# Performance work log

Hardware: AMD Instinct MI355X
Metric: run time of the kernel (lower is better)

The kernel has to match this reference:

```python
import jax, jax.numpy as jnp
import numpy as np

DIM = 384
HEADS = 6
HD = DIM // HEADS
PATCH = 2
FR = 0.5
HEXP = int(HEADS * 4.0)       # attn_proj expanded heads
PR = DIM // 4                  # SQA proj1 out dim
HID = DIM * 4                  # MLP hidden
EPS = 1e-5
SCALE = 1.0 / np.sqrt(HD).astype(np.float32)


def _ln(x, w, b):
    m = jnp.mean(x, axis=-1, keepdims=True)
    v = jnp.var(x, axis=-1, keepdims=True)
    return (x - m) / jnp.sqrt(v + EPS) * w + b


def _lin(x, w, b):
    return x @ w.T + b


def setup_inputs() -> dict:
    key = jax.random.key(0)
    ks = jax.random.split(key, 16)
    def p(i, shape, s=0.02):
        return jax.random.normal(ks[i], shape, jnp.float32) * s
    return {
        "x": jax.random.normal(ks[0], (3136, DIM), jnp.float32),
        "qa": jax.random.normal(ks[1], (1, DIM), jnp.float32),
        "conv_w": p(2, (DIM, 1, 3, 3), 0.1),
        "conv_b": jnp.zeros((DIM,), jnp.float32),
        "norm1_w": jnp.ones((DIM,), jnp.float32),
        "norm1_b": jnp.zeros((DIM,), jnp.float32),
        "norm2_w": jnp.ones((DIM,), jnp.float32),
        "norm2_b": jnp.zeros((DIM,), jnp.float32),
        "qkv_w": p(3, (3 * DIM, DIM)),
        "qkv_b": jnp.zeros((3 * DIM,), jnp.float32),
        "mproj_w": p(4, (DIM, DIM)),
        "mproj_b": jnp.zeros((DIM,), jnp.float32),
        "ap1_w": p(5, (HEXP, HEADS), 0.1),
        "ap1_b": jnp.zeros((HEXP,), jnp.float32),
        "ap2_w": p(6, (HEADS, HEXP), 0.1),
        "ap2_b": jnp.zeros((HEADS,), jnp.float32),
        "kv_w": p(7, (2 * DIM, DIM)),
        "kv_b": jnp.zeros((2 * DIM,), jnp.float32),
        "sp1_w": p(8, (PR, DIM)),
        "sp1_b": jnp.zeros((PR,), jnp.float32),
        "sp2_w": p(9, (DIM, PR)),
        "sp2_b": jnp.zeros((DIM,), jnp.float32),
        "pn_w": jnp.ones((PR,), jnp.float32),
        "pn_b": jnp.zeros((PR,), jnp.float32),
        "fc1_w": p(10, (HID, DIM)),
        "fc1_b": jnp.zeros((HID,), jnp.float32),
        "fc2_w": p(11, (DIM, HID)),
        "fc2_b": jnp.zeros((DIM,), jnp.float32),
    }


def _mmsa(x, qkv_w, qkv_b, mproj_w, mproj_b, ap1_w, ap1_b, ap2_w, ap2_b):
    # x: [S, DIM]
    s = x.shape[0]
    qkv = _lin(x, qkv_w, qkv_b).reshape(s, 3, HEADS, HD).transpose(1, 2, 0, 3)  # [3,h,s,d]
    q, k, v = qkv[0], qkv[1], qkv[2]
    attn = jnp.einsum('hqd,hkd->hqk', q, k) * SCALE           # [h,q,k]
    a = attn.transpose(1, 2, 0)                                # [q,k,h]
    a = a @ ap1_w.T + ap1_b                                    # [q,k,hexp]
    a = jax.nn.softmax(a, axis=1)                              # softmax over k (axis=1)
    a = a @ ap2_w.T + ap2_b                                    # [q,k,h]
    attn = a.transpose(2, 0, 1)                                # [h,q,k]
    out = jnp.einsum('hqk,hkd->hqd', attn, v)
    out = out.transpose(1, 0, 2).reshape(s, DIM)
    return _lin(out, mproj_w, mproj_b)


def _sqa(x, q, kv_w, kv_b, sp1_w, sp1_b, sp2_w, sp2_b, pn_w, pn_b):
    # x: [S, DIM], q: [1, DIM]
    s = x.shape[0]
    qh = q.reshape(1, HEADS, HD).transpose(1, 0, 2)            # [h,1,d]
    kv = _lin(x, kv_w, kv_b).reshape(s, 2, HEADS, HD).transpose(1, 2, 0, 3)
    k, v = kv[0], kv[1]
    attn = jax.nn.softmax(jnp.einsum('hqd,hkd->hqk', qh, k) * SCALE, axis=-1)
    x1 = jnp.einsum('hqk,hkd->hqd', attn, v).transpose(1, 0, 2).reshape(1, DIM)
    x1 = jax.nn.relu(_ln(_lin(x1, sp1_w, sp1_b), pn_w, pn_b))
    x1 = _lin(x1, sp2_w, sp2_b)
    return x + x1                                              # broadcast residual over S


def reference(x, qa, conv_w, conv_b, norm1_w, norm1_b, norm2_w, norm2_b,
              qkv_w, qkv_b, mproj_w, mproj_b, ap1_w, ap1_b, ap2_w, ap2_b,
              kv_w, kv_b, sp1_w, sp1_b, sp2_w, sp2_b, pn_w, pn_b,
              fc1_w, fc1_b, fc2_w, fc2_b):
    L = x.shape[0]
    Hs = int(np.sqrt(L)); Ws = Hs
    # PosCNN2D: depthwise 3x3 conv + residual
    xi = x.T.reshape(1, DIM, Hs, Ws)
    conv = jax.lax.conv_general_dilated(xi, conv_w, (1, 1), 'SAME', feature_group_count=DIM)
    xi = conv + conv_b[None, :, None, None] + xi
    c = xi[0]                                                  # [DIM,Hs,Ws]
    hp, wp = Hs // PATCH, Ws // PATCH
    # 'c (h h1) (w w1) -> (h w) (h1 w1) c'
    x1 = c.reshape(DIM, hp, PATCH, wp, PATCH).transpose(1, 3, 2, 4, 0).reshape(hp * wp, PATCH * PATCH, DIM)
    n = hp * wp
    nf = int(n * FR)
    means = x1.mean(axis=(1, 2))
    idx = jnp.argsort(-means)                                  # descending
    nf_idx, nb_idx = idx[:nf], idx[nf:]
    f = x1[nf_idx].reshape(nf * PATCH * PATCH, DIM)
    b = x1[nb_idx].reshape((n - nf) * PATCH * PATCH, DIM)
    qf = _mmsa(jnp.concatenate([qa, f], axis=0),
               qkv_w, qkv_b, mproj_w, mproj_b, ap1_w, ap1_b, ap2_w, ap2_b)
    qa2, f = qf[:1], qf[1:]
    b = _sqa(b, qa2, kv_w, kv_b, sp1_w, sp1_b, sp2_w, sp2_b, pn_w, pn_b)
    # scatter foreground/background back to patch order
    x1n = jnp.zeros_like(x1)
    x1n = x1n.at[nf_idx].set(f.reshape(nf, PATCH * PATCH, DIM))
    x1n = x1n.at[nb_idx].set(b.reshape(n - nf, PATCH * PATCH, DIM))
    # inverse rearrange '(h w) (h1 w1) c -> ((h h1)(w w1)) c'
    x1f = x1n.reshape(hp, wp, PATCH, PATCH, DIM).transpose(0, 2, 1, 3, 4).reshape(L, DIM)
    x = x + _ln(x1f, norm1_w, norm1_b)
    h = _ln(x, norm2_w, norm2_b)
    h = jax.nn.silu(_lin(h, fc1_w, fc1_b))
    x = x + _lin(h, fc2_w, fc2_b)
    return x, qa2
```

## Files before the change

### kernel.cpp

```cpp
#include <hip/hip_runtime.h>
#include <hip/hip_bf16.h>

#define DIM 384
#define HEADS 6
#define HD 64
#define LPIX 3136
#define HS 56
#define NPATCH 784
#define NF 392
#define SEQ 1569
#define BROWS 1568
#define HEXP 24
#define PR 96
#define HID 1536
#define SCALE 0.125f
#define EPSV 1e-5f
#define KPAD 1576
#define QSTR 9456

typedef short short8v __attribute__((ext_vector_type(8)));
typedef float f32x4 __attribute__((ext_vector_type(4)));
typedef unsigned short ushort;

__device__ __forceinline__ ushort f2b(float f) {
    __hip_bfloat16 h = __float2bfloat16(f);
    return reinterpret_cast<ushort&>(h);
}
__device__ __forceinline__ float b2f(ushort u) {
    unsigned int ui = ((unsigned int)u) << 16;
    return __uint_as_float(ui);
}

struct CvtSeg { const float* s; ushort* d; int n; };
__global__ __launch_bounds__(256) void cvt_kernel(CvtSeg a, CvtSeg b, CvtSeg c, CvtSeg d, CvtSeg e) {
    CvtSeg seg;
    switch (blockIdx.y) { case 0: seg = a; break; case 1: seg = b; break; case 2: seg = c; break;
                          case 3: seg = d; break; default: seg = e; break; }
    int idx = (blockIdx.x * 256 + threadIdx.x) * 8;
    if (idx >= seg.n) return;
    float4 f0 = *reinterpret_cast<const float4*>(seg.s + idx);
    float4 f1 = *reinterpret_cast<const float4*>(seg.s + idx + 4);
    ushort u[8] = { f2b(f0.x), f2b(f0.y), f2b(f0.z), f2b(f0.w),
                    f2b(f1.x), f2b(f1.y), f2b(f1.z), f2b(f1.w) };
    *reinterpret_cast<uint4*>(seg.d + idx) = *reinterpret_cast<uint4*>(u);
}

__global__ __launch_bounds__(384) void conv_kernel(const float* __restrict__ x,
                                                   const float* __restrict__ cw,
                                                   const float* __restrict__ cb,
                                                   float* __restrict__ x1,
                                                   float* __restrict__ means) {
    int l = blockIdx.x, c = threadIdx.x;
    int wid = c >> 6, lane = c & 63;
    int hh = l / HS, ww = l % HS;
    float acc = x[(long)l * DIM + c] + cb[c];
    #pragma unroll
    for (int kh = 0; kh < 3; kh++) {
        int h2 = hh + kh - 1;
        if (h2 < 0 || h2 >= HS) continue;
        #pragma unroll
        for (int kw = 0; kw < 3; kw++) {
            int w2 = ww + kw - 1;
            if (w2 < 0 || w2 >= HS) continue;
            acc += x[((long)h2 * HS + w2) * DIM + c] * cw[c * 9 + kh * 3 + kw];
        }
    }
    int p = (hh >> 1) * 28 + (ww >> 1);
    int t = ((hh & 1) << 1) | (ww & 1);
    x1[(long)(p * 4 + t) * DIM + c] = acc;
    float s = acc;
    #pragma unroll
    for (int off = 32; off >= 1; off >>= 1) s += __shfl_xor(s, off);
    __shared__ float wred[6];
    if (lane == 0) wred[wid] = s;
    __syncthreads();
    if (c == 0) atomicAdd(&means[p], wred[0] + wred[1] + wred[2] + wred[3] + wred[4] + wred[5]);
}

__global__ __launch_bounds__(1024) void partition_kernel(const float* __restrict__ means, int* __restrict__ isfg,
                                                         int* __restrict__ pos, int* __restrict__ fgmap,
                                                         int* __restrict__ bgmap) {
    __shared__ float m_s[NPATCH];
    __shared__ unsigned char flag_s[NPATCH];
    __shared__ int scan_s[256];
    int tid = threadIdx.x;
    if (tid < NPATCH) m_s[tid] = means[tid];
    __syncthreads();
    if (tid < NPATCH) {
        float m = m_s[tid];
        int rank = 0;
        for (int q2 = 0; q2 < NPATCH; q2++) {
            float mq = m_s[q2];
            rank += (mq > m) || (mq == m && q2 < tid);
        }
        flag_s[tid] = (rank < NF) ? 1 : 0;
    }
    __syncthreads();
    if (tid < 256) {
        int base = tid * 4, cnt = 0;
        #pragma unroll
        for (int i = 0; i < 4; i++) { int p = base + i; if (p < NPATCH) cnt += flag_s[p]; }
        scan_s[tid] = cnt;
    }
    __syncthreads();
    for (int off = 1; off < 256; off <<= 1) {
        int add = 0;
        if (tid < 256 && tid >= off) add = scan_s[tid - off];
        __syncthreads();
        if (tid < 256) scan_s[tid] += add;
        __syncthreads();
    }
    if (tid < 256) {
        int base = tid * 4, cnt = 0;
        #pragma unroll
        for (int i = 0; i < 4; i++) { int p = base + i; if (p < NPATCH) cnt += flag_s[p]; }
        int run = scan_s[tid] - cnt;
        for (int i = 0; i < 4; i++) {
            int p = base + i;
            if (p >= NPATCH) break;
            int f = flag_s[p];
            if (f) { isfg[p] = 1; pos[p] = run; fgmap[run] = p; run++; }
            else   { isfg[p] = 0; pos[p] = p - run; bgmap[p - run] = p; }
        }
    }
}

__global__ __launch_bounds__(384) void gather_kernel(const float* __restrict__ x1, const float* __restrict__ qa,
                                                     const int* __restrict__ fgmap, const int* __restrict__ bgmap,
                                                     ushort* __restrict__ Xmsa_bf, ushort* __restrict__ B_bf) {
    int c = threadIdx.x;
    int bid = blockIdx.x;
    if (bid == 0) { Xmsa_bf[c] = f2b(qa[c]); return; }
    if (bid <= BROWS) {
        int r = bid - 1;
        int src = fgmap[r >> 2] * 4 + (r & 3);
        Xmsa_bf[(long)bid * DIM + c] = f2b(x1[(long)src * DIM + c]);
    } else {
        int r = bid - SEQ;
        int src = bgmap[r >> 2] * 4 + (r & 3);
        B_bf[(long)r * DIM + c] = f2b(x1[(long)src * DIM + c]);
    }
}

template<int BM, int BN, int BK, int OPB, int ACT, int OUTBF>
__global__ __launch_bounds__(256) void mgemm(
    const ushort* __restrict__ A, int lda, long long sA,
    const ushort* __restrict__ B, int ldb, long long sB,
    const float* __restrict__ bias, const float* __restrict__ resid, int ldr,
    void* __restrict__ Cv, int ldc, long long sC,
    int M, int N, int K, float alpha) {
    constexpr int LDT = BK + 8;
    constexpr int WR = (BM == 128 && BN == 128) ? 2 : ((BM == 128) ? 4 : 2);
    constexpr int WC = 4 / WR;
    constexpr int MFR = BM / WR / 16;
    constexpr int NFR = BN / WC / 16;
    constexpr int KH = BK / 32;
    __shared__ ushort As[BM * LDT];
    __shared__ ushort Bs[BN * LDT];
    int tid = threadIdx.x;
    int wid = tid >> 6, lane = tid & 63;
    int m0 = blockIdx.y * BM, n0 = blockIdx.x * BN;
    int bz = blockIdx.z;
    A += (long long)bz * sA;
    B += (long long)bz * sB;
    int wm = (wid / WC) * (BM / WR);
    int wn = (wid % WC) * (BN / WC);
    f32x4 acc[MFR][NFR];
    #pragma unroll
    for (int mi = 0; mi < MFR; mi++)
        #pragma unroll
        for (int ni = 0; ni < NFR; ni++) acc[mi][ni] = (f32x4){0.f, 0.f, 0.f, 0.f};

    for (int k0 = 0; k0 < K; k0 += BK) {
        {
            constexpr int CPR = BK / 8;
            constexpr int CHA = BM * CPR / 256;
            #pragma unroll
            for (int t = 0; t < CHA; t++) {
                int chunk = tid + t * 256;
                int row = chunk / CPR, part = chunk % CPR;
                int gm = m0 + row, gk = k0 + part * 8;
                ushort* dst = &As[row * LDT + part * 8];
                if (gm < M && gk + 8 <= K) {
                    *reinterpret_cast<uint4*>(dst) =
                        *reinterpret_cast<const uint4*>(&A[(long long)gm * lda + gk]);
                } else {
                    #pragma unroll
                    for (int i = 0; i < 8; i++) {
                        int k = gk + i;
                        dst[i] = (gm < M && k < K) ? A[(long long)gm * lda + k] : (ushort)0;
                    }
                }
            }
        }
        if (OPB == 1) {
            constexpr int CPR = BK / 8;
            constexpr int CHB = BN * CPR / 256;
            #pragma unroll
            for (int t = 0; t < CHB; t++) {
                int chunk = tid + t * 256;
                int row = chunk / CPR, part = chunk % CPR;
                int gn = n0 + row, gk = k0 + part * 8;
                ushort* dst = &Bs[row * LDT + part * 8];
                if (gn < N && gk + 8 <= K) {
                    *reinterpret_cast<uint4*>(dst) =
                        *reinterpret_cast<const uint4*>(&B[(long long)gn * ldb + gk]);
                } else {
                    #pragma unroll
                    for (int i = 0; i < 8; i++) {
                        int k = gk + i;
                        dst[i] = (gn < N && k < K) ? B[(long long)gn * ldb + k] : (ushort)0;
                    }
                }
            }
        } else {
            int kr = tid >> 2, nn = (tid & 3) * 16;
            int gk = k0 + kr;
            ushort vals[16];
            if (gk < K && n0 + nn + 16 <= N) {
                *reinterpret_cast<uint4*>(vals) =
                    *reinterpret_cast<const uint4*>(&B[(long long)gk * ldb + n0 + nn]);
                *reinterpret_cast<uint4*>(vals + 8) =
                    *reinterpret_cast<const uint4*>(&B[(long long)gk * ldb + n0 + nn + 8]);
            } else {
                #pragma unroll
                for (int i = 0; i < 16; i++) {
                    int gn = n0 + nn + i;
                    vals[i] = (gk < K && gn < N) ? B[(long long)gk * ldb + gn] : (ushort)0;
                }
            }
            #pragma unroll
            for (int i = 0; i < 16; i++) Bs[(nn + i) * LDT + kr] = vals[i];
        }
        __syncthreads();
        #pragma unroll
        for (int kh = 0; kh < KH; kh++) {
            short8v a[MFR], b[NFR];
            int kcol = kh * 32 + (lane >> 4) * 8;
            #pragma unroll
            for (int mi = 0; mi < MFR; mi++)
                a[mi] = *reinterpret_cast<const short8v*>(&As[(wm + mi * 16 + (lane & 15)) * LDT + kcol]);
            #pragma unroll
            for (int ni = 0; ni < NFR; ni++)
                b[ni] = *reinterpret_cast<const short8v*>(&Bs[(wn + ni * 16 + (lane & 15)) * LDT + kcol]);
            #pragma unroll
            for (int mi = 0; mi < MFR; mi++)
                #pragma unroll
                for (int ni = 0; ni < NFR; ni++)
                    acc[mi][ni] = __builtin_amdgcn_mfma_f32_16x16x32_bf16(a[mi], b[ni], acc[mi][ni], 0, 0, 0);
        }
        __syncthreads();
    }
    ushort* C16 = (ushort*)Cv;
    float* C32 = (float*)Cv;
    #pragma unroll
    for (int mi = 0; mi < MFR; mi++) {
        #pragma unroll
        for (int j = 0; j < 4; j++) {
            int gm = m0 + wm + mi * 16 + (lane >> 4) * 4 + j;
            if (gm >= M) continue;
            #pragma unroll
            for (int ni = 0; ni < NFR; ni++) {
                int gn = n0 + wn + ni * 16 + (lane & 15);
                if (gn >= N) continue;
                float v = acc[mi][ni][j] * alpha;
                if (bias) v += bias[gn];
                if (ACT == 1) v = v / (1.f + __expf(-v));
                if (resid) v += resid[(long long)gm * ldr + gn];
                long long ci = bz * sC + (long long)gm * ldc + gn;
                if (OUTBF) C16[ci] = f2b(v); else C32[ci] = v;
            }
        }
    }
}

__global__ __launch_bounds__(512, 2) void modattn_kernel(
    ushort* __restrict__ S,
    const float* __restrict__ ap1_w, const float* __restrict__ ap1_b,
    const float* __restrict__ ap2_w, const float* __restrict__ ap2_b) {
    int q = blockIdx.x, tid = threadIdx.x;
    int wid = tid >> 6, lane = tid & 63;
    __shared__ ushort s_lds[6 * KPAD];
    __shared__ float w1s[144], w2s[144], b1s[24], b2s[6];
    __shared__ float red[8][12];
    __shared__ float fin[12];
    if (tid < 144) { w1s[tid] = ap1_w[tid]; w2s[tid] = ap2_w[tid]; }
    if (tid < 24) b1s[tid] = ap1_b[tid];
    if (tid < 6)  b2s[tid] = ap2_b[tid];
    {
        const uint4* g = reinterpret_cast<const uint4*>(S + (long long)q * QSTR);
        uint4* l = reinterpret_cast<uint4*>(s_lds);
        #pragma unroll
        for (int t = 0; t < 3; t++) {
            int i = tid + t * 512;
            if (i < 1182) l[i] = g[i];
        }
    }
    __syncthreads();
    float a2acc[4][6];
    #pragma unroll
    for (int j = 0; j < 4; j++)
        #pragma unroll
        for (int h = 0; h < 6; h++) a2acc[j][h] = b2s[h];

    #pragma unroll
    for (int c = 0; c < 2; c++) {
        float a1[4][12];
        float r12[12];
        #pragma unroll
        for (int e = 0; e < 12; e++) r12[e] = -3.4e38f;
        #pragma unroll
        for (int j = 0; j < 4; j++) {
            int k = tid + j * 512;
            bool val = k < SEQ;
            int kc = val ? k : 0;
            float sv[6];
            #pragma unroll
            for (int h = 0; h < 6; h++) sv[h] = b2f(s_lds[h * KPAD + kc]);
            #pragma unroll
            for (int e = 0; e < 12; e++) {
                int eg = c * 12 + e;
                float a = b1s[eg];
                #pragma unroll
                for (int h = 0; h < 6; h++) a = fmaf(sv[h], w1s[eg * 6 + h], a);
                a1[j][e] = a;
                if (val) r12[e] = fmaxf(r12[e], a);
            }
        }
        #pragma unroll
        for (int e = 0; e < 12; e++) {
            float v = r12[e];
            #pragma unroll
            for (int off = 32; off >= 1; off >>= 1) v = fmaxf(v, __shfl_xor(v, off));
            r12[e] = v;
        }
        if (lane == 0) {
            #pragma unroll
            for (int e = 0; e < 12; e++) red[wid][e] = r12[e];
        }
        __syncthreads();
        if (tid < 12) {
            float v = red[0][tid];
            #pragma unroll
            for (int w = 1; w < 8; w++) v = fmaxf(v, red[w][tid]);
            fin[tid] = v;
        }
        __syncthreads();
        #pragma unroll
        for (int e = 0; e < 12; e++) r12[e] = 0.f;
        #pragma unroll
        for (int j = 0; j < 4; j++) {
            int k = tid + j * 512;
            bool val = k < SEQ;
            #pragma unroll
            for (int e = 0; e < 12; e++) {
                float p = val ? __expf(a1[j][e] - fin[e]) : 0.f;
                a1[j][e] = p;
                r12[e] += p;
            }
        }
        #pragma unroll
        for (int e = 0; e < 12; e++) {
            float v = r12[e];
            #pragma unroll
            for (int off = 32; off >= 1; off >>= 1) v += __shfl_xor(v, off);
            r12[e] = v;
        }
        if (lane == 0) {
            #pragma unroll
            for (int e = 0; e < 12; e++) red[wid][e] = r12[e];
        }
        __syncthreads();
        if (tid < 12) {
            float v = red[0][tid];
            #pragma unroll
            for (int w = 1; w < 8; w++) v += red[w][tid];
            fin[tid] = 1.f / v;
        }
        __syncthreads();
        #pragma unroll
        for (int j = 0; j < 4; j++) {
            #pragma unroll
            for (int e = 0; e < 12; e++) {
                float p = a1[j][e] * fin[e];
                int eg = c * 12 + e;
                #pragma unroll
                for (int h = 0; h < 6; h++) a2acc[j][h] = fmaf(p, w2s[h * 24 + eg], a2acc[j][h]);
            }
        }
    }
    #pragma unroll
    for (int j = 0; j < 4; j++) {
        int k = tid + j * 512;
        if (k < SEQ) {
            #pragma unroll
            for (int h = 0; h < 6; h++) s_lds[h * KPAD + k] = f2b(a2acc[j][h]);
        } else if (k < KPAD) {
            #pragma unroll
            for (int h = 0; h < 6; h++) s_lds[h * KPAD + k] = 0;
        }
    }
    __syncthreads();
    {
        const uint4* l = reinterpret_cast<const uint4*>(s_lds);
        uint4* g = reinterpret_cast<uint4*>(S + (long long)q * QSTR);
        #pragma unroll
        for (int t = 0; t < 3; t++) {
            int i = tid + t * 512;
            if (i < 1182) g[i] = l[i];
        }
    }
}

__global__ __launch_bounds__(512) void sqa_attn_kernel(const float* __restrict__ kv, const float* __restrict__ qa2,
                                                       float* __restrict__ x1h) {
    int h = blockIdx.x, tid = threadIdx.x;
    int wid = tid >> 6, lane = tid & 63;
    __shared__ float q_s[HD];
    __shared__ float l_s[BROWS];
    __shared__ float red8[8];
    __shared__ float pvred[8][HD];
    __shared__ float gmv;
    if (tid < HD) q_s[tid] = qa2[h * HD + tid];
    __syncthreads();
    float lmax = -1e30f;
    #pragma unroll
    for (int j = 0; j < 4; j++) {
        int s = tid + j * 512;
        if (s < BROWS) {
            const float4* kr = reinterpret_cast<const float4*>(kv + (long long)s * 768 + h * HD);
            float d = 0.f;
            #pragma unroll
            for (int i = 0; i < 16; i++) {
                float4 f = kr[i];
                d = fmaf(f.x, q_s[i * 4 + 0], d); d = fmaf(f.y, q_s[i * 4 + 1], d);
                d = fmaf(f.z, q_s[i * 4 + 2], d); d = fmaf(f.w, q_s[i * 4 + 3], d);
            }
            d *= SCALE;
            l_s[s] = d;
            lmax = fmaxf(lmax, d);
        }
    }
    #pragma unroll
    for (int off = 32; off >= 1; off >>= 1) lmax = fmaxf(lmax, __shfl_xor(lmax, off));
    if (lane == 0) red8[wid] = lmax;
    __syncthreads();
    if (tid == 0) {
        float v = red8[0];
        #pragma unroll
        for (int w = 1; w < 8; w++) v = fmaxf(v, red8[w]);
        gmv = v;
    }
    __syncthreads();
    float gmax = gmv;
    float lsum = 0.f;
    #pragma unroll
    for (int j = 0; j < 4; j++) {
        int s = tid + j * 512;
        if (s < BROWS) { float pp = __expf(l_s[s] - gmax); l_s[s] = pp; lsum += pp; }
    }
    #pragma unroll
    for (int off = 32; off >= 1; off >>= 1) lsum += __shfl_xor(lsum, off);
    if (lane == 0) red8[wid] = lsum;
    __syncthreads();
    if (tid == 0) {
        float v = 0.f;
        #pragma unroll
        for (int w = 0; w < 8; w++) v += red8[w];
        gmv = 1.f / v;
    }
    __syncthreads();
    float inv = gmv;
    int d = tid & 63, g = tid >> 6;
    float acc = 0.f;
    for (int s = g; s < BROWS; s += 8)
        acc = fmaf(l_s[s], kv[(long long)s * 768 + 384 + h * HD + d], acc);
    pvred[g][d] = acc;
    __syncthreads();
    if (tid < HD) {
        float v = 0.f;
        #pragma unroll
        for (int w = 0; w < 8; w++) v += pvred[w][tid];
        x1h[h * HD + tid] = v * inv;
    }
}

__global__ __launch_bounds__(384) void sqa_mlp_kernel(const float* __restrict__ x1h,
                                                      const float* __restrict__ sp1_w, const float* __restrict__ sp1_b,
                                                      const float* __restrict__ pn_w, const float* __restrict__ pn_b,
                                                      const float* __restrict__ sp2_w, const float* __restrict__ sp2_b,
                                                      float* __restrict__ z,
                                                      const float* __restrict__ mp, float* __restrict__ dq) {
    __shared__ float y_s[PR];
    __shared__ float x_s[DIM];
    __shared__ float mv[2];
    int tid = threadIdx.x;
    dq[tid] = mp[tid];
    x_s[tid] = x1h[tid];
    __syncthreads();
    if (tid < PR) {
        float a = sp1_b[tid];
        for (int c = 0; c < DIM; c++) a += sp1_w[tid * DIM + c] * x_s[c];
        y_s[tid] = a;
    }
    __syncthreads();
    if (tid == 0) {
        float m = 0.f; for (int i = 0; i < PR; i++) m += y_s[i]; m /= (float)PR;
        float v = 0.f; for (int i = 0; i < PR; i++) { float d = y_s[i] - m; v += d * d; } v /= (float)PR;
        mv[0] = m; mv[1] = rsqrtf(v + EPSV);
    }
    __syncthreads();
    if (tid < PR) {
        float yn = (y_s[tid] - mv[0]) * mv[1] * pn_w[tid] + pn_b[tid];
        y_s[tid] = fmaxf(yn, 0.f);
    }
    __syncthreads();
    float a = sp2_b[tid];
    for (int j = 0; j < PR; j++) a += sp2_w[tid * PR + j] * y_s[j];
    z[tid] = a;
}

__global__ __launch_bounds__(384) void scatter_ln_kernel(
    const float* __restrict__ x, const float* __restrict__ mpout, const ushort* __restrict__ B_bf,
    const float* __restrict__ z, const int* __restrict__ isfg, const int* __restrict__ pos,
    const float* __restrict__ n1w, const float* __restrict__ n1b,
    const float* __restrict__ n2w, const float* __restrict__ n2b,
    float* __restrict__ x_mid, ushort* __restrict__ hnorm_bf) {
    int l = blockIdx.x, c = threadIdx.x;
    int wid = c >> 6, lane = c & 63;
    int hh = l / HS, ww = l % HS;
    int p = (hh >> 1) * 28 + (ww >> 1);
    int t = ((hh & 1) << 1) | (ww & 1);
    float v;
    if (isfg[p]) v = mpout[(long long)(1 + pos[p] * 4 + t) * DIM + c];
    else v = b2f(B_bf[(long long)(pos[p] * 4 + t) * DIM + c]) + z[c];
    __shared__ float r0[8], r1[8], r2[8], r3[8];
    float s1 = v, s2 = v * v;
    #pragma unroll
    for (int off = 32; off >= 1; off >>= 1) { s1 += __shfl_xor(s1, off); s2 += __shfl_xor(s2, off); }
    if (lane == 0) { r0[wid] = s1; r1[wid] = s2; }
    __syncthreads();
    float mean = (r0[0] + r0[1] + r0[2] + r0[3] + r0[4] + r0[5]) / (float)DIM;
    float var = (r1[0] + r1[1] + r1[2] + r1[3] + r1[4] + r1[5]) / (float)DIM - mean * mean;
    float xm = x[(long long)l * DIM + c] + (v - mean) * rsqrtf(var + EPSV) * n1w[c] + n1b[c];
    x_mid[(long long)l * DIM + c] = xm;
    s1 = xm; s2 = xm * xm;
    #pragma unroll
    for (int off = 32; off >= 1; off >>= 1) { s1 += __shfl_xor(s1, off); s2 += __shfl_xor(s2, off); }
    if (lane == 0) { r2[wid] = s1; r3[wid] = s2; }
    __syncthreads();
    float m2 = (r2[0] + r2[1] + r2[2] + r2[3] + r2[4] + r2[5]) / (float)DIM;
    float v2 = (r3[0] + r3[1] + r3[2] + r3[3] + r3[4] + r3[5]) / (float)DIM - m2 * m2;
    hnorm_bf[(long long)l * DIM + c] = f2b((xm - m2) * rsqrtf(v2 + EPSV) * n2w[c] + n2b[c]);
}

extern "C" void kernel_launch(void* const* d_in, const int* in_sizes, int n_in,
                              void* d_out, int out_size, void* d_ws, size_t ws_size,
                              hipStream_t stream) {
    const float* x       = (const float*)d_in[0];
    const float* qa      = (const float*)d_in[1];
    const float* conv_w  = (const float*)d_in[2];
    const float* conv_b  = (const float*)d_in[3];
    const float* n1w     = (const float*)d_in[4];
    const float* n1b     = (const float*)d_in[5];
    const float* n2w     = (const float*)d_in[6];
    const float* n2b     = (const float*)d_in[7];
    const float* qkv_w   = (const float*)d_in[8];
    const float* qkv_b   = (const float*)d_in[9];
    const float* mproj_w = (const float*)d_in[10];
    const float* mproj_b = (const float*)d_in[11];
    const float* ap1_w   = (const float*)d_in[12];
    const float* ap1_b   = (const float*)d_in[13];
    const float* ap2_w   = (const float*)d_in[14];
    const float* ap2_b   = (const float*)d_in[15];
    const float* kv_w    = (const float*)d_in[16];
    const float* kv_b    = (const float*)d_in[17];
    const float* sp1_w   = (const float*)d_in[18];
    const float* sp1_b   = (const float*)d_in[19];
    const float* sp2_w   = (const float*)d_in[20];
    const float* sp2_b   = (const float*)d_in[21];
    const float* pn_w    = (const float*)d_in[22];
    const float* pn_b    = (const float*)d_in[23];
    const float* fc1_w   = (const float*)d_in[24];
    const float* fc1_b   = (const float*)d_in[25];
    const float* fc2_w   = (const float*)d_in[26];
    const float* fc2_b   = (const float*)d_in[27];
    float* out = (float*)d_out;
    float* ws  = (float*)d_ws;

    const long long X1_OFF    = 0;
    const long long BMAT_OFF  = 1204224;
    const long long S_OFF     = 1806336;
    const long long MPOUT_OFF = 16576912;
    const long long XMID_OFF  = 17179408;
    const long long WBF_OFF   = 18383632;
    const long long MEANS_OFF = 19415824;
    const long long X1H_OFF   = 19416608;
    const long long Z_OFF     = 19416992;
    const long long ISFG_OFF  = 19418160;
    const long long POS_OFF   = 19418944;
    const long long FGMAP_OFF = 19419728;
    const long long BGMAP_OFF = 19420120;

    float*  x1_arr  = ws + X1_OFF;
    float*  mpout   = ws + MPOUT_OFF;
    float*  xmid    = ws + XMID_OFF;
    float*  means   = ws + MEANS_OFF;
    float*  x1h     = ws + X1H_OFF;
    float*  zvec    = ws + Z_OFF;
    int*    isfg    = (int*)(ws + ISFG_OFF);
    int*    pos     = (int*)(ws + POS_OFF);
    int*    fgmap   = (int*)(ws + FGMAP_OFF);
    int*    bgmap   = (int*)(ws + BGMAP_OFF);

    ushort* S16     = (ushort*)(ws + S_OFF);
    ushort* qkvb_bf = (ushort*)(ws + X1_OFF);
    ushort* Xmsa_bf = (ushort*)(ws + MPOUT_OFF);
    ushort* Bmat_bf = (ushort*)(ws + BMAT_OFF);
    ushort* attn_bf = (ushort*)(ws + XMID_OFF);
    float*  kv_out  = ws + S_OFF;
    ushort* hnorm_bf= (ushort*)(ws + S_OFF + 1204224);
    ushort* hact_bf = (ushort*)(ws + S_OFF + 1806336);

    ushort* wbf      = (ushort*)(ws + WBF_OFF);
    ushort* qkvw_bf  = wbf;
    ushort* mprojw_bf= wbf + 442368;
    ushort* kvw_bf   = wbf + 589824;
    ushort* fc1w_bf  = wbf + 884736;
    ushort* fc2w_bf  = wbf + 1474560;

    {
        CvtSeg s0{qkv_w, qkvw_bf, 442368};
        CvtSeg s1{mproj_w, mprojw_bf, 147456};
        CvtSeg s2{kv_w, kvw_bf, 294912};
        CvtSeg s3{fc1_w, fc1w_bf, 589824};
        CvtSeg s4{fc2_w, fc2w_bf, 589824};
        dim3 g(288, 5, 1);
        cvt_kernel<<<g, 256, 0, stream>>>(s0, s1, s2, s3, s4);
    }

    hipMemsetAsync(means, 0, NPATCH * sizeof(float), stream);
    conv_kernel<<<LPIX, 384, 0, stream>>>(x, conv_w, conv_b, x1_arr, means);
    partition_kernel<<<1, 1024, 0, stream>>>(means, isfg, pos, fgmap, bgmap);
    gather_kernel<<<SEQ + BROWS, 384, 0, stream>>>(x1_arr, qa, fgmap, bgmap, Xmsa_bf, Bmat_bf);

    {
        dim3 g(18, 25, 1);
        mgemm<64,64,64,1,0,1><<<g, 256, 0, stream>>>(Xmsa_bf, DIM, 0, qkvw_bf, DIM, 0, qkv_b,
                                                     nullptr, 0, qkvb_bf, 1152, 0, SEQ, 1152, DIM, 1.f);
    }
    {
        dim3 g(13, 13, 6);
        mgemm<128,128,64,1,0,1><<<g, 256, 0, stream>>>(qkvb_bf, 1152, 64, qkvb_bf + 384, 1152, 64, nullptr,
                                                       nullptr, 0, S16, QSTR, (long long)KPAD, SEQ, SEQ, HD, SCALE);
    }
    modattn_kernel<<<SEQ, 512, 0, stream>>>(S16, ap1_w, ap1_b, ap2_w, ap2_b);
    {
        dim3 g(1, 25, 6);
        mgemm<64,64,64,0,0,1><<<g, 256, 0, stream>>>(S16, QSTR, (long long)KPAD, qkvb_bf + 768, 1152, 64, nullptr,
                                                     nullptr, 0, attn_bf, DIM, 64, SEQ, HD, SEQ, 1.f);
    }
    {
        dim3 g(6, 25, 1);
        mgemm<64,64,64,1,0,0><<<g, 256, 0, stream>>>(attn_bf, DIM, 0, mprojw_bf, DIM, 0, mproj_b,
                                                     nullptr, 0, mpout, DIM, 0, SEQ, DIM, DIM, 1.f);
    }
    {
        dim3 g(12, 25, 1);
        mgemm<64,64,64,1,0,0><<<g, 256, 0, stream>>>(Bmat_bf, DIM, 0, kvw_bf, DIM, 0, kv_b,
                                                     nullptr, 0, kv_out, 768, 0, BROWS, 768, DIM, 1.f);
    }
    sqa_attn_kernel<<<HEADS, 512, 0, stream>>>(kv_out, mpout , x1h);
    sqa_mlp_kernel<<<1, 384, 0, stream>>>(x1h, sp1_w, sp1_b, pn_w, pn_b, sp2_w, sp2_b, zvec,
                                          mpout, out + (long long)LPIX * DIM);
    scatter_ln_kernel<<<LPIX, 384, 0, stream>>>(x, mpout, Bmat_bf, zvec, isfg, pos,
                                                n1w, n1b, n2w, n2b, xmid, hnorm_bf);
    {
        dim3 g(12, 25, 1);
        mgemm<128,128,64,1,1,1><<<g, 256, 0, stream>>>(hnorm_bf, DIM, 0, fc1w_bf, DIM, 0, fc1_b,
                                                       nullptr, 0, hact_bf, HID, 0, LPIX, HID, DIM, 1.f);
    }
    {
        dim3 g(6, 50, 1);
        mgemm<64,64,64,1,0,0><<<g, 256, 0, stream>>>(hact_bf, HID, 0, fc2w_bf, HID, 0, fc2_b,
                                                     xmid, DIM, out, DIM, 0, LPIX, DIM, HID, 1.f);
    }
}
```

Baseline: 556.8 us.

## Split-K the PV GEMM with atomics, merge mproj and kv GEMMs, retile fc1

The attention-times-V GEMM had only 150 blocks. It is now split four ways along K, with atomic fp32 accumulation into a zeroed buffer, followed by a separate bf16 conversion kernel. The mproj and kv projection GEMMs are merged into one dual-dispatch launch to cut launch overhead and fill more CUs. fc1 moves from 128x128 to 64x64 tiles for more blocks, and the fc2 grid is trimmed to the exact row count. The cost is an extra memset, a conversion pass, atomic traffic, and nondeterministic summation order.

```diff
diff --git a/kernel.cpp b/kernel.cpp
--- a/kernel.cpp
+++ b/kernel.cpp
@@ -45,6 +45,16 @@
     *reinterpret_cast<uint4*>(seg.d + idx) = *reinterpret_cast<uint4*>(u);
 }
 
+__global__ __launch_bounds__(256) void cvtattn_kernel(const float* __restrict__ s, ushort* __restrict__ d) {
+    int idx = (blockIdx.x * 256 + threadIdx.x) * 8;
+    if (idx >= SEQ * DIM) return;
+    float4 f0 = *reinterpret_cast<const float4*>(s + idx);
+    float4 f1 = *reinterpret_cast<const float4*>(s + idx + 4);
+    ushort u[8] = { f2b(f0.x), f2b(f0.y), f2b(f0.z), f2b(f0.w),
+                    f2b(f1.x), f2b(f1.y), f2b(f1.z), f2b(f1.w) };
+    *reinterpret_cast<uint4*>(d + idx) = *reinterpret_cast<uint4*>(u);
+}
+
 __global__ __launch_bounds__(384) void conv_kernel(const float* __restrict__ x,
                                                    const float* __restrict__ cw,
                                                    const float* __restrict__ cb,
@@ -142,27 +152,25 @@
     }
 }
 
-template<int BM, int BN, int BK, int OPB, int ACT, int OUTBF>
-__global__ __launch_bounds__(256) void mgemm(
-    const ushort* __restrict__ A, int lda, long long sA,
-    const ushort* __restrict__ B, int ldb, long long sB,
-    const float* __restrict__ bias, const float* __restrict__ resid, int ldr,
-    void* __restrict__ Cv, int ldc, long long sC,
-    int M, int N, int K, float alpha) {
+struct GArgs {
+    const ushort* A; int lda;
+    const ushort* B; int ldb;
+    const float* bias; const float* resid; int ldr;
+    void* C; int ldc;
+    int M, N, K; float alpha;
+};
+
+template<int BM, int BN, int BK, int OPB, int ACT, int OUTBF, int ATOMIC>
+__device__ __forceinline__ void gemm_tile(const GArgs g, int bx, int by, ushort* As, ushort* Bs) {
     constexpr int LDT = BK + 8;
     constexpr int WR = (BM == 128 && BN == 128) ? 2 : ((BM == 128) ? 4 : 2);
     constexpr int WC = 4 / WR;
     constexpr int MFR = BM / WR / 16;
     constexpr int NFR = BN / WC / 16;
     constexpr int KH = BK / 32;
-    __shared__ ushort As[BM * LDT];
-    __shared__ ushort Bs[BN * LDT];
     int tid = threadIdx.x;
     int wid = tid >> 6, lane = tid & 63;
-    int m0 = blockIdx.y * BM, n0 = blockIdx.x * BN;
-    int bz = blockIdx.z;
-    A += (long long)bz * sA;
-    B += (long long)bz * sB;
+    int m0 = by * BM, n0 = bx * BN;
     int wm = (wid / WC) * (BM / WR);
     int wn = (wid % WC) * (BN / WC);
     f32x4 acc[MFR][NFR];
@@ -171,7 +179,7 @@
         #pragma unroll
         for (int ni = 0; ni < NFR; ni++) acc[mi][ni] = (f32x4){0.f, 0.f, 0.f, 0.f};
 
-    for (int k0 = 0; k0 < K; k0 += BK) {
+    for (int k0 = 0; k0 < g.K; k0 += BK) {
         {
             constexpr int CPR = BK / 8;
             constexpr int CHA = BM * CPR / 256;
@@ -181,14 +189,14 @@
                 int row = chunk / CPR, part = chunk % CPR;
                 int gm = m0 + row, gk = k0 + part * 8;
                 ushort* dst = &As[row * LDT + part * 8];
-                if (gm < M && gk + 8 <= K) {
+                if (gm < g.M && gk + 8 <= g.K) {
                     *reinterpret_cast<uint4*>(dst) =
-                        *reinterpret_cast<const uint4*>(&A[(long long)gm * lda + gk]);
+                        *reinterpret_cast<const uint4*>(&g.A[(long long)gm * g.lda + gk]);
                 } else {
                     #pragma unroll
                     for (int i = 0; i < 8; i++) {
                         int k = gk + i;
-                        dst[i] = (gm < M && k < K) ? A[(long long)gm * lda + k] : (ushort)0;
+                        dst[i] = (gm < g.M && k < g.K) ? g.A[(long long)gm * g.lda + k] : (ushort)0;
                     }
                 }
             }
@@ -202,14 +210,14 @@
                 int row = chunk / CPR, part = chunk % CPR;
                 int gn = n0 + row, gk = k0 + part * 8;
                 ushort* dst = &Bs[row * LDT + part * 8];
-                if (gn < N && gk + 8 <= K) {
+                if (gn < g.N && gk + 8 <= g.K) {
                     *reinterpret_cast<uint4*>(dst) =
-                        *reinterpret_cast<const uint4*>(&B[(long long)gn * ldb + gk]);
+                        *reinterpret_cast<const uint4*>(&g.B[(long long)gn * g.ldb + gk]);
                 } else {
                     #pragma unroll
                     for (int i = 0; i < 8; i++) {
                         int k = gk + i;
-                        dst[i] = (gn < N && k < K) ? B[(long long)gn * ldb + k] : (ushort)0;
+                        dst[i] = (gn < g.N && k < g.K) ? g.B[(long long)gn * g.ldb + k] : (ushort)0;
                     }
                 }
             }
@@ -217,16 +225,16 @@
             int kr = tid >> 2, nn = (tid & 3) * 16;
             int gk = k0 + kr;
             ushort vals[16];
-            if (gk < K && n0 + nn + 16 <= N) {
+            if (gk < g.K && n0 + nn + 16 <= g.N) {
                 *reinterpret_cast<uint4*>(vals) =
-                    *reinterpret_cast<const uint4*>(&B[(long long)gk * ldb + n0 + nn]);
+                    *reinterpret_cast<const uint4*>(&g.B[(long long)gk * g.ldb + n0 + nn]);
                 *reinterpret_cast<uint4*>(vals + 8) =
-                    *reinterpret_cast<const uint4*>(&B[(long long)gk * ldb + n0 + nn + 8]);
+                    *reinterpret_cast<const uint4*>(&g.B[(long long)gk * g.ldb + n0 + nn + 8]);
             } else {
                 #pragma unroll
                 for (int i = 0; i < 16; i++) {
                     int gn = n0 + nn + i;
-                    vals[i] = (gk < K && gn < N) ? B[(long long)gk * ldb + gn] : (ushort)0;
+                    vals[i] = (gk < g.K && gn < g.N) ? g.B[(long long)gk * g.ldb + gn] : (ushort)0;
                 }
             }
             #pragma unroll
@@ -251,27 +259,74 @@
         }
         __syncthreads();
     }
-    ushort* C16 = (ushort*)Cv;
-    float* C32 = (float*)Cv;
+    ushort* C16 = (ushort*)g.C;
+    float* C32 = (float*)g.C;
     #pragma unroll
     for (int mi = 0; mi < MFR; mi++) {
         #pragma unroll
         for (int j = 0; j < 4; j++) {
             int gm = m0 + wm + mi * 16 + (lane >> 4) * 4 + j;
-            if (gm >= M) continue;
+            if (gm >= g.M) continue;
             #pragma unroll
             for (int ni = 0; ni < NFR; ni++) {
                 int gn = n0 + wn + ni * 16 + (lane & 15);
-                if (gn >= N) continue;
-                float v = acc[mi][ni][j] * alpha;
-                if (bias) v += bias[gn];
-                if (ACT == 1) v = v / (1.f + __expf(-v));
-                if (resid) v += resid[(long long)gm * ldr + gn];
-                long long ci = bz * sC + (long long)gm * ldc + gn;
-                if (OUTBF) C16[ci] = f2b(v); else C32[ci] = v;
+                if (gn >= g.N) continue;
+                float v = acc[mi][ni][j] * g.alpha;
+                long long ci = (long long)gm * g.ldc + gn;
+                if (ATOMIC) {
+                    atomicAdd(&C32[ci], v);
+                } else {
+                    if (g.bias) v += g.bias[gn];
+                    if (ACT == 1) v = v / (1.f + __expf(-v));
+                    if (g.resid) v += g.resid[(long long)gm * g.ldr + gn];
+                    if (OUTBF) C16[ci] = f2b(v); else C32[ci] = v;
+                }
             }
         }
     }
+}
+
+template<int BM, int BN, int BK, int OPB, int ACT, int OUTBF>
+__global__ __launch_bounds__(256) void mgemm(
+    const ushort* A, int lda, long long sA,
+    const ushort* B, int ldb, long long sB,
+    const float* bias, const float* resid, int ldr,
+    void* Cv, int ldc, long long sC,
+    int M, int N, int K, float alpha) {
+    __shared__ ushort As[BM * (BK + 8)];
+    __shared__ ushort Bs[BN * (BK + 8)];
+    GArgs g;
+    g.A = A + (long long)blockIdx.z * sA; g.lda = lda;
+    g.B = B + (long long)blockIdx.z * sB; g.ldb = ldb;
+    g.bias = bias; g.resid = resid; g.ldr = ldr;
+    g.C = OUTBF ? (void*)((ushort*)Cv + (long long)blockIdx.z * sC)
+                : (void*)((float*)Cv + (long long)blockIdx.z * sC);
+    g.ldc = ldc; g.M = M; g.N = N; g.K = K; g.alpha = alpha;
+    gemm_tile<BM, BN, BK, OPB, ACT, OUTBF, 0>(g, blockIdx.x, blockIdx.y, As, Bs);
+}
+
+__global__ __launch_bounds__(256) void mgemm_dual(GArgs a, GArgs b, int xsplit) {
+    __shared__ ushort As[64 * 72];
+    __shared__ ushort Bs[64 * 72];
+    if ((int)blockIdx.x < xsplit) gemm_tile<64, 64, 64, 1, 0, 0, 0>(a, blockIdx.x, blockIdx.y, As, Bs);
+    else                          gemm_tile<64, 64, 64, 1, 0, 0, 0>(b, blockIdx.x - xsplit, blockIdx.y, As, Bs);
+}
+
+__global__ __launch_bounds__(256) void pv_kernel(const ushort* __restrict__ S16, const ushort* __restrict__ V,
+                                                 float* __restrict__ attn_f32) {
+    __shared__ ushort As[64 * 72];
+    __shared__ ushort Bs[64 * 72];
+    int z = blockIdx.z;
+    int h = z >> 2, ks = z & 3;
+    int kbeg = ks * 400;
+    int kend = (kbeg + 400 < SEQ) ? kbeg + 400 : SEQ;
+    GArgs g;
+    g.A = S16 + h * KPAD + kbeg; g.lda = QSTR;
+    g.B = V + h * HD + (long long)kbeg * 1152; g.ldb = 1152;
+    g.bias = nullptr; g.resid = nullptr; g.ldr = 0;
+    g.C = attn_f32 + h * HD; g.ldc = DIM;
+    g.M = SEQ; g.N = HD; g.K = kend - kbeg; g.alpha = 1.f;
+    gemm_tile<64, 64, 64, 0, 0, 0, 1>(g, 0, blockIdx.y, As, Bs);
 }
 
 __global__ __launch_bounds__(512, 2) void modattn_kernel(
@@ -617,7 +672,8 @@
     ushort* qkvb_bf = (ushort*)(ws + X1_OFF);
     ushort* Xmsa_bf = (ushort*)(ws + MPOUT_OFF);
     ushort* Bmat_bf = (ushort*)(ws + BMAT_OFF);
-    ushort* attn_bf = (ushort*)(ws + XMID_OFF);
+    float*  attn_f32= ws + XMID_OFF;
+    ushort* attn_bf = (ushort*)(ws + XMID_OFF + 602496);
     float*  kv_out  = ws + S_OFF;
     ushort* hnorm_bf= (ushort*)(ws + S_OFF + 1204224);
     ushort* hact_bf = (ushort*)(ws + S_OFF + 1806336);
@@ -640,6 +696,7 @@
     }
 
     hipMemsetAsync(means, 0, NPATCH * sizeof(float), stream);
+    hipMemsetAsync(attn_f32, 0, (size_t)SEQ * DIM * sizeof(float), stream);
     conv_kernel<<<LPIX, 384, 0, stream>>>(x, conv_w, conv_b, x1_arr, means);
     partition_kernel<<<1, 1024, 0, stream>>>(means, isfg, pos, fgmap, bgmap);
     gather_kernel<<<SEQ + BROWS, 384, 0, stream>>>(x1_arr, qa, fgmap, bgmap, Xmsa_bf, Bmat_bf);
@@ -656,19 +713,21 @@
     }
     modattn_kernel<<<SEQ, 512, 0, stream>>>(S16, ap1_w, ap1_b, ap2_w, ap2_b);
     {
-        dim3 g(1, 25, 6);
-        mgemm<64,64,64,0,0,1><<<g, 256, 0, stream>>>(S16, QSTR, (long long)KPAD, qkvb_bf + 768, 1152, 64, nullptr,
-                                                     nullptr, 0, attn_bf, DIM, 64, SEQ, HD, SEQ, 1.f);
-    }
-    {
-        dim3 g(6, 25, 1);
-        mgemm<64,64,64,1,0,0><<<g, 256, 0, stream>>>(attn_bf, DIM, 0, mprojw_bf, DIM, 0, mproj_b,
-                                                     nullptr, 0, mpout, DIM, 0, SEQ, DIM, DIM, 1.f);
-    }
-    {
-        dim3 g(12, 25, 1);
-        mgemm<64,64,64,1,0,0><<<g, 256, 0, stream>>>(Bmat_bf, DIM, 0, kvw_bf, DIM, 0, kv_b,
-                                                     nullptr, 0, kv_out, 768, 0, BROWS, 768, DIM, 1.f);
+        dim3 g(1, 25, 24);
+        pv_kernel<<<g, 256, 0, stream>>>(S16, qkvb_bf + 768, attn_f32);
+    }
+    cvtattn_kernel<<<295, 256, 0, stream>>>(attn_f32, attn_bf);
+    {
+        GArgs gm_;
+        gm_.A = attn_bf; gm_.lda = DIM; gm_.B = mprojw_bf; gm_.ldb = DIM;
+        gm_.bias = mproj_b; gm_.resid = nullptr; gm_.ldr = 0;
+        gm_.C = mpout; gm_.ldc = DIM; gm_.M = SEQ; gm_.N = DIM; gm_.K = DIM; gm_.alpha = 1.f;
+        GArgs gk_;
+        gk_.A = Bmat_bf; gk_.lda = DIM; gk_.B = kvw_bf; gk_.ldb = DIM;
+        gk_.bias = kv_b; gk_.resid = nullptr; gk_.ldr = 0;
+        gk_.C = kv_out; gk_.ldc = 768; gk_.M = BROWS; gk_.N = 768; gk_.K = DIM; gk_.alpha = 1.f;
+        dim3 g(18, 25, 1);
+        mgemm_dual<<<g, 256, 0, stream>>>(gm_, gk_, 6);
     }
     sqa_attn_kernel<<<HEADS, 512, 0, stream>>>(kv_out, mpout , x1h);
     sqa_mlp_kernel<<<1, 384, 0, stream>>>(x1h, sp1_w, sp1_b, pn_w, pn_b, sp2_w, sp2_b, zvec,
@@ -676,12 +735,12 @@
     scatter_ln_kernel<<<LPIX, 384, 0, stream>>>(x, mpout, Bmat_bf, zvec, isfg, pos,
                                                 n1w, n1b, n2w, n2b, xmid, hnorm_bf);
     {
-        dim3 g(12, 25, 1);
-        mgemm<128,128,64,1,1,1><<<g, 256, 0, stream>>>(hnorm_bf, DIM, 0, fc1w_bf, DIM, 0, fc1_b,
-                                                       nullptr, 0, hact_bf, HID, 0, LPIX, HID, DIM, 1.f);
-    }
-    {
-        dim3 g(6, 50, 1);
+        dim3 g(24, 49, 1);
+        mgemm<64,64,64,1,1,1><<<g, 256, 0, stream>>>(hnorm_bf, DIM, 0, fc1w_bf, DIM, 0, fc1_b,
+                                                     nullptr, 0, hact_bf, HID, 0, LPIX, HID, DIM, 1.f);
+    }
+    {
+        dim3 g(6, 49, 1);
         mgemm<64,64,64,1,0,0><<<g, 256, 0, stream>>>(hact_bf, HID, 0, fc2w_bf, HID, 0, fc2_b,
                                                      xmid, DIM, out, DIM, 0, LPIX, DIM, HID, 1.f);
     }
```

New measurement: 507.8 us. 1.1x faster.
